# Kernel optimization log

Measured on AMD Instinct MI355X. Metric: run time of the kernel, lower is better.

## Reference

```python
import jax, jax.numpy as jnp
import numpy as np

D_MODEL = 1024
N_HEADS = 16


def setup_inputs() -> dict:
    key = jax.random.key(0)
    k1, k2, k3 = jax.random.split(key, 3)
    B, S = 2, 2048
    std_qkv = (2.0 / (D_MODEL + 3 * D_MODEL)) ** 0.5
    std_out = (2.0 / (D_MODEL + D_MODEL)) ** 0.5
    X = jax.random.normal(k1, (B, S, D_MODEL), dtype=jnp.float32)
    W_qkv = jax.random.normal(k2, (3 * D_MODEL, D_MODEL), dtype=jnp.float32) * std_qkv
    W_out = jax.random.normal(k3, (D_MODEL, D_MODEL), dtype=jnp.float32) * std_out
    return {"X": X, "W_qkv": W_qkv, "W_out": W_out}


def reference(X, W_qkv, W_out):
    B, S, D = X.shape
    H = N_HEADS
    dk = D // H
    # qkv projection: (..., d) @ W^T -> (..., 3d)
    qkv = jnp.einsum('bsd,ed->bse', X, W_qkv)
    Q, K, V = jnp.split(qkv, 3, axis=-1)
    # split heads: (B, S, H*dk) -> (B, H, S, dk)
    def heads(t):
        return t.reshape(B, S, H, dk).transpose(0, 2, 1, 3)
    Q, K, V = heads(Q), heads(K), heads(V)
    # scaled scores (B, H, S, S)
    scores = jnp.einsum('bhqd,bhkd->bhqk', Q, K) / jnp.sqrt(jnp.float32(dk))
    causal = jnp.tril(jnp.ones((S, S), dtype=bool))
    scores = jnp.where(causal, scores.astype(jnp.float32), -jnp.inf)
    weights = jax.nn.softmax(scores, axis=-1).astype(X.dtype)
    out = jnp.einsum('bhqk,bhkd->bhqd', weights, V)
    out = out.transpose(0, 2, 1, 3).reshape(B, S, D)
    return jnp.einsum('bsd,od->bso', out, W_out)
```

## Files before the change

### kernel.cpp

```cpp
#include <hip/hip_runtime.h>

typedef __bf16 bf16;
typedef __bf16 bf16x4v __attribute__((ext_vector_type(4)));
typedef __bf16 bf16x8 __attribute__((ext_vector_type(8)));
typedef float f32x4 __attribute__((ext_vector_type(4)));

#define MFMA16(a, b, c) __builtin_amdgcn_mfma_f32_16x16x32_bf16((a), (b), (c), 0, 0, 0)

#if __has_builtin(__builtin_amdgcn_exp2f)
#define EXP2(x) __builtin_amdgcn_exp2f(x)
#else
#define EXP2(x) exp2f(x)
#endif

#define SEQ 2048
#define DM 1024
#define NH 16

typedef __attribute__((address_space(3))) unsigned int lds_u32;
typedef __attribute__((address_space(1))) const unsigned int glb_u32;

__device__ __forceinline__ void gld16(const bf16* g, bf16* l) {
    __builtin_amdgcn_global_load_lds((glb_u32*)g, (lds_u32*)l, 16, 0, 0);
}

__global__ __launch_bounds__(256) void cvt_all(const float* __restrict__ X,
                                               const float* __restrict__ Wq,
                                               const float* __restrict__ Wo,
                                               bf16* __restrict__ Xb,
                                               bf16* __restrict__ Wqb,
                                               bf16* __restrict__ Wob) {
    const int i = blockIdx.x * 256 + threadIdx.x;
    const int N1 = (4 * 1024 * 1024) / 4;
    const int N2 = (3 * 1024 * 1024) / 4;
    const float* s; bf16* d; int off;
    if (i < N1)            { s = X;  d = Xb;  off = i; }
    else if (i < N1 + N2)  { s = Wq; d = Wqb; off = i - N1; }
    else                   { s = Wo; d = Wob; off = i - N1 - N2; }
    const float4 v = ((const float4*)s)[off];
    bf16x4v o;
    o.x = (bf16)v.x; o.y = (bf16)v.y; o.z = (bf16)v.z; o.w = (bf16)v.w;
    ((bf16x4v*)d)[off] = o;
}

__global__ __launch_bounds__(256) void gemm_qkv(const bf16* __restrict__ A,
                                                const bf16* __restrict__ B,
                                                bf16* __restrict__ qkbuf,
                                                bf16* __restrict__ vtg) {
    __shared__ bf16 smem[16384];
    bf16* As = smem;
    bf16* Bs = smem + 8192;

    const int K = DM, tid = threadIdx.x;
    const int lane = tid & 63, w = tid >> 6;
    const int quad = lane >> 4, l15 = lane & 15;
    const int wm = (w & 1) * 64, wn = (w >> 1) * 64;
    const int rowBase = blockIdx.y * 128, colBase = blockIdx.x * 128;

    f32x4 acc[4][4] = {};

    for (int k0 = 0; k0 < K; k0 += 64) {
        __syncthreads();
#pragma unroll
        for (int i = 0; i < 4; ++i) {
            const int c = i * 256 + tid;
            const int row = c >> 3;
            const int sg = (c & 7) ^ (row & 7);
            gld16(A + (size_t)(rowBase + row) * K + k0 + sg * 8,
                  As + (i * 256 + w * 64) * 8);
            gld16(B + (size_t)(colBase + row) * K + k0 + sg * 8,
                  Bs + (i * 256 + w * 64) * 8);
        }
        __syncthreads();

#pragma unroll
        for (int ks = 0; ks < 2; ++ks) {
            bf16x8 af[4], bfr[4];
#pragma unroll
            for (int i = 0; i < 4; ++i) {
                const int ra = wm + i * 16 + l15;
                af[i]  = *(const bf16x8*)(As + ra * 64 + (((ks * 4 + quad) ^ (ra & 7)) * 8));
                const int rb = wn + i * 16 + l15;
                bfr[i] = *(const bf16x8*)(Bs + rb * 64 + (((ks * 4 + quad) ^ (rb & 7)) * 8));
            }
#pragma unroll
            for (int i = 0; i < 4; ++i)
#pragma unroll
                for (int j = 0; j < 4; ++j)
                    acc[i][j] = MFMA16(af[i], bfr[j], acc[i][j]);
        }
    }

    if (colBase < 2 * DM) {
#pragma unroll
        for (int i = 0; i < 4; ++i)
#pragma unroll
            for (int j = 0; j < 4; ++j)
#pragma unroll
                for (int r = 0; r < 4; ++r)
                    qkbuf[(size_t)(rowBase + wm + i * 16 + quad * 4 + r) * 2048 +
                          colBase + wn + j * 16 + l15] = (bf16)acc[i][j][r];
    } else {
        bf16* T = smem;
        const int vcolBase = colBase - 2 * DM;
        const int bb = rowBase >> 11;
        const int sBase = rowBase & 2047;
        const int drow0 = tid >> 4, seg = tid & 15;
#pragma unroll
        for (int c = 0; c < 2; ++c) {
            __syncthreads();
            if ((w >> 1) == c) {
#pragma unroll
                for (int i = 0; i < 4; ++i)
#pragma unroll
                    for (int j = 0; j < 4; ++j) {
                        bf16x4v pk;
#pragma unroll
                        for (int r = 0; r < 4; ++r) pk[r] = (bf16)acc[i][j][r];
                        *(bf16x4v*)(T + (j * 16 + l15) * 136 + wm + i * 16 + quad * 4) = pk;
                    }
            }
            __syncthreads();
#pragma unroll
            for (int rr = 0; rr < 4; ++rr) {
                const int drow = rr * 16 + drow0;
                *(bf16x8*)(vtg + (size_t)(bb * DM + vcolBase + c * 64 + drow) * SEQ +
                           sBase + seg * 8) =
                    *(const bf16x8*)(T + drow * 136 + seg * 8);
            }
        }
    }
}

__global__ __launch_bounds__(256) void gemm_out(const bf16* __restrict__ A,
                                                const bf16* __restrict__ B,
                                                float* __restrict__ C) {
    __shared__ bf16 As[64 * 64];
    __shared__ bf16 Bs[128 * 64];

    const int K = DM, N = DM, tid = threadIdx.x;
    const int lane = tid & 63, w = tid >> 6;
    const int quad = lane >> 4, l15 = lane & 15;
    const int wm = (w & 1) * 32, wn = (w >> 1) * 64;
    const int rowBase = blockIdx.y * 64, colBase = blockIdx.x * 128;

    f32x4 acc[2][4] = {};

    for (int k0 = 0; k0 < K; k0 += 64) {
        __syncthreads();
#pragma unroll
        for (int i = 0; i < 2; ++i) {
            const int c = i * 256 + tid;
            const int row = c >> 3;
            const int sg = (c & 7) ^ (row & 7);
            gld16(A + (size_t)(rowBase + row) * K + k0 + sg * 8,
                  As + (i * 256 + w * 64) * 8);
        }
#pragma unroll
        for (int i = 0; i < 4; ++i) {
            const int c = i * 256 + tid;
            const int row = c >> 3;
            const int sg = (c & 7) ^ (row & 7);
            gld16(B + (size_t)(colBase + row) * K + k0 + sg * 8,
                  Bs + (i * 256 + w * 64) * 8);
        }
        __syncthreads();

#pragma unroll
        for (int ks = 0; ks < 2; ++ks) {
            bf16x8 af[2], bfr[4];
#pragma unroll
            for (int i = 0; i < 2; ++i) {
                const int ra = wm + i * 16 + l15;
                af[i] = *(const bf16x8*)(As + ra * 64 + (((ks * 4 + quad) ^ (ra & 7)) * 8));
            }
#pragma unroll
            for (int j = 0; j < 4; ++j) {
                const int rb = wn + j * 16 + l15;
                bfr[j] = *(const bf16x8*)(Bs + rb * 64 + (((ks * 4 + quad) ^ (rb & 7)) * 8));
            }
#pragma unroll
            for (int i = 0; i < 2; ++i)
#pragma unroll
                for (int j = 0; j < 4; ++j)
                    acc[i][j] = MFMA16(af[i], bfr[j], acc[i][j]);
        }
    }

#pragma unroll
    for (int i = 0; i < 2; ++i)
#pragma unroll
        for (int j = 0; j < 4; ++j)
#pragma unroll
            for (int r = 0; r < 4; ++r)
                C[(size_t)(rowBase + wm + i * 16 + quad * 4 + r) * N +
                  colBase + wn + j * 16 + l15] = acc[i][j][r];
}

__global__ __launch_bounds__(128) void attn_fwd(const bf16* __restrict__ qk,
                                                const bf16* __restrict__ vtg,
                                                bf16* __restrict__ ao) {
    __shared__ bf16 Ks[64 * 72];
    __shared__ bf16 Vts[64 * 72];
    __shared__ bf16 Pb[2][2][16 * 72];

    const int tid = threadIdx.x;
    const int lane = tid & 63, w = tid >> 6;
    const int quad = lane >> 4, l15 = lane & 15;
    const int bh = blockIdx.x;
    const int b = bh >> 4, h = bh & 15;
    const int lo = blockIdx.y;
    const int hi = 63 - lo;
    const int g0 = lo * 32 + w * 16;
    const int g1 = hi * 32 + w * 16;

    const bf16* qkb   = qk + (size_t)b * SEQ * 2048;
    const bf16* kbase = qkb + DM + h * 64;
    const bf16* vb    = vtg + (size_t)bh * 64 * SEQ;

    const float SC = 0.125f * 1.44269504f;
    bf16x8 q0lo, q0hi, q1lo, q1hi;
    {
        const bf16* qp0 = qkb + (size_t)(g0 + l15) * 2048 + h * 64 + quad * 8;
        const bf16* qp1 = qkb + (size_t)(g1 + l15) * 2048 + h * 64 + quad * 8;
        bf16x8 a0 = *(const bf16x8*)qp0, c0 = *(const bf16x8*)(qp0 + 32);
        bf16x8 a1 = *(const bf16x8*)qp1, c1 = *(const bf16x8*)(qp1 + 32);
#pragma unroll
        for (int i = 0; i < 8; ++i) {
            q0lo[i] = (bf16)((float)a0[i] * SC);
            q0hi[i] = (bf16)((float)c0[i] * SC);
            q1lo[i] = (bf16)((float)a1[i] * SC);
            q1hi[i] = (bf16)((float)c1[i] * SC);
        }
    }

    f32x4 o0[4] = {}, o1[4] = {};
    float l0 = 0.f, l1 = 0.f;

    const int nkt = (hi + 2) >> 1;
    for (int kt = 0; kt < nkt; ++kt) {
        const int k0 = kt * 64;
        __syncthreads();
#pragma unroll
        for (int i = 0; i < 4; ++i) {
            const int c = i * 128 + tid, kr = c >> 3, sg = c & 7;
            *(bf16x8*)(Ks + kr * 72 + sg * 8) =
                *(const bf16x8*)(kbase + (size_t)(k0 + kr) * 2048 + sg * 8);
            *(bf16x8*)(Vts + kr * 72 + sg * 8) =
                *(const bf16x8*)(vb + (size_t)kr * SEQ + k0 + sg * 8);
        }
        __syncthreads();

        const bool live0 = (k0 <= g0 + 15);
        f32x4 s0[4], s1[4];
#pragma unroll
        for (int t = 0; t < 4; ++t) {
            const bf16* kp = Ks + (t * 16 + l15) * 72 + quad * 8;
            bf16x8 klo = *(const bf16x8*)kp;
            bf16x8 khi = *(const bf16x8*)(kp + 32);
            f32x4 z = {};
            z = MFMA16(klo, q1lo, z);
            z = MFMA16(khi, q1hi, z);
            s1[t] = z;
            if (live0) {
                f32x4 y = {};
                y = MFMA16(klo, q0lo, y);
                y = MFMA16(khi, q0hi, y);
                s0[t] = y;
            }
        }

        auto sfm = [&](f32x4* s, int g, float& li, bf16* P) {
            if (k0 + 63 > g) {
#pragma unroll
                for (int t = 0; t < 4; ++t)
#pragma unroll
                    for (int r = 0; r < 4; ++r)
                        if (k0 + t * 16 + quad * 4 + r > g + l15) s[t][r] = -1e30f;
            }
#pragma unroll
            for (int t = 0; t < 4; ++t) {
                bf16x4v pb4;
#pragma unroll
                for (int r = 0; r < 4; ++r) {
                    const float p = EXP2(s[t][r]);
                    li += p;
                    pb4[r] = (bf16)p;
                }
                *(bf16x4v*)(P + l15 * 72 + t * 16 + quad * 4) = pb4;
            }
        };

        sfm(s1, g1, l1, &Pb[w][1][0]);
        if (live0) sfm(s0, g0, l0, &Pb[w][0][0]);

        asm volatile("s_waitcnt lgkmcnt(0)" ::: "memory");
        bf16x8 p1a = *(const bf16x8*)(&Pb[w][1][0] + l15 * 72 + quad * 8);
        bf16x8 p1b = *(const bf16x8*)(&Pb[w][1][0] + l15 * 72 + 32 + quad * 8);
        bf16x8 p0a, p0b;
        if (live0) {
            p0a = *(const bf16x8*)(&Pb[w][0][0] + l15 * 72 + quad * 8);
            p0b = *(const bf16x8*)(&Pb[w][0][0] + l15 * 72 + 32 + quad * 8);
        }

#pragma unroll
        for (int dt = 0; dt < 4; ++dt) {
            const bf16* vp = Vts + (dt * 16 + l15) * 72 + quad * 8;
            bf16x8 v0 = *(const bf16x8*)vp;
            bf16x8 v1 = *(const bf16x8*)(vp + 32);
            o1[dt] = MFMA16(v0, p1a, o1[dt]);
            o1[dt] = MFMA16(v1, p1b, o1[dt]);
            if (live0) {
                o0[dt] = MFMA16(v0, p0a, o0[dt]);
                o0[dt] = MFMA16(v1, p0b, o0[dt]);
            }
        }
    }

    l0 += __shfl_xor(l0, 16); l0 += __shfl_xor(l0, 32);
    l1 += __shfl_xor(l1, 16); l1 += __shfl_xor(l1, 32);

    const float i0 = 1.f / l0, i1 = 1.f / l1;
    bf16* a0 = ao + (size_t)(b * SEQ + g0 + l15) * DM + h * 64;
    bf16* a1 = ao + (size_t)(b * SEQ + g1 + l15) * DM + h * 64;
#pragma unroll
    for (int dt = 0; dt < 4; ++dt) {
        bf16x4v v0, v1;
#pragma unroll
        for (int r = 0; r < 4; ++r) {
            v0[r] = (bf16)(o0[dt][r] * i0);
            v1[r] = (bf16)(o1[dt][r] * i1);
        }
        *(bf16x4v*)(a0 + dt * 16 + quad * 4) = v0;
        *(bf16x4v*)(a1 + dt * 16 + quad * 4) = v1;
    }
}

extern "C" void kernel_launch(void* const* d_in, const int* in_sizes, int n_in,
                              void* d_out, int out_size, void* d_ws, size_t ws_size,
                              hipStream_t stream) {
    const float* X    = (const float*)d_in[0];
    const float* Wqkv = (const float*)d_in[1];
    const float* Wout = (const float*)d_in[2];
    float* out = (float*)d_out;

    const int M = 2 * SEQ;
    const size_t nX    = (size_t)M * DM;
    const size_t nWqkv = (size_t)3 * DM * DM;
    const size_t nWout = (size_t)DM * DM;
    const size_t nQK   = (size_t)M * 2 * DM;
    const size_t nVT   = (size_t)2 * DM * SEQ;
    const size_t nAO   = (size_t)M * DM;

    if (ws_size < (nX + nWqkv + nWout + nQK + nVT + nAO) * sizeof(bf16)) return;

    bf16* Xb    = (bf16*)d_ws;
    bf16* Wqkvb = Xb + nX;
    bf16* Woutb = Wqkvb + nWqkv;
    bf16* qkbuf = Woutb + nWout;
    bf16* vtg   = qkbuf + nQK;
    bf16* ao    = vtg + nVT;

    const int nCvt4 = (int)((nX + nWqkv + nWout) / 4);
    cvt_all<<<dim3(nCvt4 / 256), 256, 0, stream>>>(X, Wqkv, Wout, Xb, Wqkvb, Woutb);

    gemm_qkv<<<dim3(3 * DM / 128, M / 128), 256, 0, stream>>>(Xb, Wqkvb, qkbuf, vtg);
    attn_fwd<<<dim3(2 * NH, SEQ / 64), 128, 0, stream>>>(qkbuf, vtg, ao);
    gemm_out<<<dim3(DM / 128, M / 64), 256, 0, stream>>>(ao, Woutb, out);
}
```

Measured before the change: 181.8 us.

## Double query rows per attention block and load K/V tiles via swizzled global_load_lds

Each attention block now handles 128 query rows (two 64-row tiles paired lo/hi for causal balance) instead of 64, so every K/V tile loaded into LDS serves twice as many queries. K/V staging switches from register round-trips to direct global-to-LDS loads with an XOR-swizzled, unpadded layout to avoid bank conflicts. Masking is limited to the diagonal tile per group. The change halves the grid and raises register pressure (16 accumulator tiles), which may reduce occupancy.

```diff
diff --git a/kernel.cpp b/kernel.cpp
--- a/kernel.cpp
+++ b/kernel.cpp
@@ -200,9 +200,9 @@
 __global__ __launch_bounds__(128) void attn_fwd(const bf16* __restrict__ qk,
                                                 const bf16* __restrict__ vtg,
                                                 bf16* __restrict__ ao) {
-    __shared__ bf16 Ks[64 * 72];
-    __shared__ bf16 Vts[64 * 72];
-    __shared__ bf16 Pb[2][2][16 * 72];
+    __shared__ bf16 Ks[64 * 64];
+    __shared__ bf16 Vts[64 * 64];
+    __shared__ bf16 Pb[2][4][16 * 72];
 
     const int tid = threadIdx.x;
     const int lane = tid & 63, w = tid >> 6;
@@ -210,129 +210,133 @@
     const int bh = blockIdx.x;
     const int b = bh >> 4, h = bh & 15;
     const int lo = blockIdx.y;
-    const int hi = 63 - lo;
-    const int g0 = lo * 32 + w * 16;
-    const int g1 = hi * 32 + w * 16;
+    const int hi = 31 - lo;
+    const int nkt = hi + 1;
 
     const bf16* qkb   = qk + (size_t)b * SEQ * 2048;
     const bf16* kbase = qkb + DM + h * 64;
     const bf16* vb    = vtg + (size_t)bh * 64 * SEQ;
 
+    int qs[4];
+    qs[0] = hi * 64 + w * 32;  qs[1] = qs[0] + 16;
+    qs[2] = lo * 64 + w * 32;  qs[3] = qs[2] + 16;
+
     const float SC = 0.125f * 1.44269504f;
-    bf16x8 q0lo, q0hi, q1lo, q1hi;
-    {
-        const bf16* qp0 = qkb + (size_t)(g0 + l15) * 2048 + h * 64 + quad * 8;
-        const bf16* qp1 = qkb + (size_t)(g1 + l15) * 2048 + h * 64 + quad * 8;
-        bf16x8 a0 = *(const bf16x8*)qp0, c0 = *(const bf16x8*)(qp0 + 32);
-        bf16x8 a1 = *(const bf16x8*)qp1, c1 = *(const bf16x8*)(qp1 + 32);
+    bf16x8 qfl[4], qfh[4];
+#pragma unroll
+    for (int g = 0; g < 4; ++g) {
+        const bf16* qp = qkb + (size_t)(qs[g] + l15) * 2048 + h * 64 + quad * 8;
+        bf16x8 a = *(const bf16x8*)qp;
+        bf16x8 c = *(const bf16x8*)(qp + 32);
 #pragma unroll
         for (int i = 0; i < 8; ++i) {
-            q0lo[i] = (bf16)((float)a0[i] * SC);
-            q0hi[i] = (bf16)((float)c0[i] * SC);
-            q1lo[i] = (bf16)((float)a1[i] * SC);
-            q1hi[i] = (bf16)((float)c1[i] * SC);
-        }
-    }
-
-    f32x4 o0[4] = {}, o1[4] = {};
-    float l0 = 0.f, l1 = 0.f;
-
-    const int nkt = (hi + 2) >> 1;
+            qfl[g][i] = (bf16)((float)a[i] * SC);
+            qfh[g][i] = (bf16)((float)c[i] * SC);
+        }
+    }
+
+    f32x4 o[4][4] = {};
+    float lsum[4] = {0.f, 0.f, 0.f, 0.f};
+
     for (int kt = 0; kt < nkt; ++kt) {
         const int k0 = kt * 64;
         __syncthreads();
 #pragma unroll
         for (int i = 0; i < 4; ++i) {
-            const int c = i * 128 + tid, kr = c >> 3, sg = c & 7;
-            *(bf16x8*)(Ks + kr * 72 + sg * 8) =
-                *(const bf16x8*)(kbase + (size_t)(k0 + kr) * 2048 + sg * 8);
-            *(bf16x8*)(Vts + kr * 72 + sg * 8) =
-                *(const bf16x8*)(vb + (size_t)kr * SEQ + k0 + sg * 8);
-        }
-        __syncthreads();
-
-        const bool live0 = (k0 <= g0 + 15);
-        f32x4 s0[4], s1[4];
+            const int c = i * 128 + tid;
+            const int row = c >> 3;
+            const int sg = (c & 7) ^ (row & 7);
+            gld16(kbase + (size_t)(k0 + row) * 2048 + sg * 8,
+                  Ks + (i * 128 + w * 64) * 8);
+            gld16(vb + (size_t)row * SEQ + k0 + sg * 8,
+                  Vts + (i * 128 + w * 64) * 8);
+        }
+        __syncthreads();
+
+        const bool liveA = (kt <= lo);
+        const bool mA = (kt == lo);
+        const bool mB = (kt == nkt - 1);
+
+        bf16x8 fr[8];
 #pragma unroll
         for (int t = 0; t < 4; ++t) {
-            const bf16* kp = Ks + (t * 16 + l15) * 72 + quad * 8;
-            bf16x8 klo = *(const bf16x8*)kp;
-            bf16x8 khi = *(const bf16x8*)(kp + 32);
-            f32x4 z = {};
-            z = MFMA16(klo, q1lo, z);
-            z = MFMA16(khi, q1hi, z);
-            s1[t] = z;
-            if (live0) {
-                f32x4 y = {};
-                y = MFMA16(klo, q0lo, y);
-                y = MFMA16(khi, q0hi, y);
-                s0[t] = y;
-            }
-        }
-
-        auto sfm = [&](f32x4* s, int g, float& li, bf16* P) {
-            if (k0 + 63 > g) {
-#pragma unroll
-                for (int t = 0; t < 4; ++t)
-#pragma unroll
-                    for (int r = 0; r < 4; ++r)
-                        if (k0 + t * 16 + quad * 4 + r > g + l15) s[t][r] = -1e30f;
-            }
-#pragma unroll
-            for (int t = 0; t < 4; ++t) {
-                bf16x4v pb4;
-#pragma unroll
-                for (int r = 0; r < 4; ++r) {
-                    const float p = EXP2(s[t][r]);
-                    li += p;
-                    pb4[r] = (bf16)p;
+            const int rk = t * 16 + l15;
+            fr[2 * t]     = *(const bf16x8*)(Ks + rk * 64 + ((quad ^ (rk & 7)) * 8));
+            fr[2 * t + 1] = *(const bf16x8*)(Ks + rk * 64 + (((4 + quad) ^ (rk & 7)) * 8));
+        }
+
+#pragma unroll
+        for (int g = 0; g < 4; ++g) {
+            if (g < 2 || liveA) {
+                f32x4 s[4];
+#pragma unroll
+                for (int t = 0; t < 4; ++t) {
+                    f32x4 z = {};
+                    z = MFMA16(fr[2 * t], qfl[g], z);
+                    z = MFMA16(fr[2 * t + 1], qfh[g], z);
+                    s[t] = z;
                 }
-                *(bf16x4v*)(P + l15 * 72 + t * 16 + quad * 4) = pb4;
-            }
-        };
-
-        sfm(s1, g1, l1, &Pb[w][1][0]);
-        if (live0) sfm(s0, g0, l0, &Pb[w][0][0]);
-
+                const bool dm = (g < 2) ? mB : mA;
+                if (dm) {
+#pragma unroll
+                    for (int t = 0; t < 4; ++t)
+#pragma unroll
+                        for (int r = 0; r < 4; ++r)
+                            if (k0 + t * 16 + quad * 4 + r > qs[g] + l15)
+                                s[t][r] = -1e30f;
+                }
+                bf16* P = &Pb[w][g][0];
+#pragma unroll
+                for (int t = 0; t < 4; ++t) {
+                    bf16x4v p4;
+#pragma unroll
+                    for (int r = 0; r < 4; ++r) {
+                        const float p = EXP2(s[t][r]);
+                        lsum[g] += p;
+                        p4[r] = (bf16)p;
+                    }
+                    *(bf16x4v*)(P + l15 * 72 + t * 16 + quad * 4) = p4;
+                }
+            }
+        }
+
+#pragma unroll
+        for (int t = 0; t < 4; ++t) {
+            const int rv = t * 16 + l15;
+            fr[2 * t]     = *(const bf16x8*)(Vts + rv * 64 + ((quad ^ (rv & 7)) * 8));
+            fr[2 * t + 1] = *(const bf16x8*)(Vts + rv * 64 + (((4 + quad) ^ (rv & 7)) * 8));
+        }
         asm volatile("s_waitcnt lgkmcnt(0)" ::: "memory");
-        bf16x8 p1a = *(const bf16x8*)(&Pb[w][1][0] + l15 * 72 + quad * 8);
-        bf16x8 p1b = *(const bf16x8*)(&Pb[w][1][0] + l15 * 72 + 32 + quad * 8);
-        bf16x8 p0a, p0b;
-        if (live0) {
-            p0a = *(const bf16x8*)(&Pb[w][0][0] + l15 * 72 + quad * 8);
-            p0b = *(const bf16x8*)(&Pb[w][0][0] + l15 * 72 + 32 + quad * 8);
-        }
-
+
+#pragma unroll
+        for (int g = 0; g < 4; ++g) {
+            if (g < 2 || liveA) {
+                const bf16* P = &Pb[w][g][0];
+                bf16x8 pa = *(const bf16x8*)(P + l15 * 72 + quad * 8);
+                bf16x8 pb = *(const bf16x8*)(P + l15 * 72 + 32 + quad * 8);
+#pragma unroll
+                for (int dt = 0; dt < 4; ++dt) {
+                    o[g][dt] = MFMA16(fr[2 * dt], pa, o[g][dt]);
+                    o[g][dt] = MFMA16(fr[2 * dt + 1], pb, o[g][dt]);
+                }
+            }
+        }
+    }
+
+#pragma unroll
+    for (int g = 0; g < 4; ++g) {
+        float lg = lsum[g];
+        lg += __shfl_xor(lg, 16);
+        lg += __shfl_xor(lg, 32);
+        const float inv = 1.f / lg;
+        bf16* ap = ao + (size_t)(b * SEQ + qs[g] + l15) * DM + h * 64;
 #pragma unroll
         for (int dt = 0; dt < 4; ++dt) {
-            const bf16* vp = Vts + (dt * 16 + l15) * 72 + quad * 8;
-            bf16x8 v0 = *(const bf16x8*)vp;
-            bf16x8 v1 = *(const bf16x8*)(vp + 32);
-            o1[dt] = MFMA16(v0, p1a, o1[dt]);
-            o1[dt] = MFMA16(v1, p1b, o1[dt]);
-            if (live0) {
-                o0[dt] = MFMA16(v0, p0a, o0[dt]);
-                o0[dt] = MFMA16(v1, p0b, o0[dt]);
-            }
-        }
-    }
-
-    l0 += __shfl_xor(l0, 16); l0 += __shfl_xor(l0, 32);
-    l1 += __shfl_xor(l1, 16); l1 += __shfl_xor(l1, 32);
-
-    const float i0 = 1.f / l0, i1 = 1.f / l1;
-    bf16* a0 = ao + (size_t)(b * SEQ + g0 + l15) * DM + h * 64;
-    bf16* a1 = ao + (size_t)(b * SEQ + g1 + l15) * DM + h * 64;
-#pragma unroll
-    for (int dt = 0; dt < 4; ++dt) {
-        bf16x4v v0, v1;
-#pragma unroll
-        for (int r = 0; r < 4; ++r) {
-            v0[r] = (bf16)(o0[dt][r] * i0);
-            v1[r] = (bf16)(o1[dt][r] * i1);
-        }
-        *(bf16x4v*)(a0 + dt * 16 + quad * 4) = v0;
-        *(bf16x4v*)(a1 + dt * 16 + quad * 4) = v1;
+            bf16x4v ov;
+#pragma unroll
+            for (int r = 0; r < 4; ++r) ov[r] = (bf16)(o[g][dt][r] * inv);
+            *(bf16x4v*)(ap + dt * 16 + quad * 4) = ov;
+        }
     }
 }
 
@@ -365,6 +369,6 @@
     cvt_all<<<dim3(nCvt4 / 256), 256, 0, stream>>>(X, Wqkv, Wout, Xb, Wqkvb, Woutb);
 
     gemm_qkv<<<dim3(3 * DM / 128, M / 128), 256, 0, stream>>>(Xb, Wqkvb, qkbuf, vtg);
-    attn_fwd<<<dim3(2 * NH, SEQ / 64), 128, 0, stream>>>(qkbuf, vtg, ao);
+    attn_fwd<<<dim3(2 * NH, SEQ / 128), 128, 0, stream>>>(qkbuf, vtg, ao);
     gemm_out<<<dim3(DM / 128, M / 64), 256, 0, stream>>>(ao, Woutb, out);
 }
```

After: 183.9 us. No clear change (+1.2%).
